# Performance work log

Measured on AMD Instinct MI355X. Metric: run time of the kernel, lower is better.

Reference implementation:

```python
import jax, jax.numpy as jnp
import numpy as np

B, S, D, H = 2, 2048, 1024, 16
Dh = D // H
EPS = 1e-6


def _layernorm(x, alpha, beta):
    # torch.std is unbiased (ddof=1); module divides by (std + eps)
    m = jnp.mean(x, axis=-1, keepdims=True)
    var = jnp.sum((x - m) ** 2, axis=-1, keepdims=True) / (x.shape[-1] - 1)
    return alpha * (x - m) / (jnp.sqrt(var) + EPS) + beta


def setup_inputs() -> dict:
    key = jax.random.key(0)
    ks = jax.random.split(key, 12)
    sc = 0.02
    return {
        "x": jax.random.normal(ks[0], (B, S, D), jnp.float32),
        "src_mask": jnp.ones((B, 1, S), jnp.int32),
        # per-head q/k/v projections stacked over heads: [H, D, Dh]
        "Wq": jax.random.normal(ks[1], (H, D, Dh), jnp.float32) * sc,
        "bq": jnp.zeros((H, Dh), jnp.float32),
        "Wk": jax.random.normal(ks[2], (H, D, Dh), jnp.float32) * sc,
        "bk": jnp.zeros((H, Dh), jnp.float32),
        "Wv": jax.random.normal(ks[3], (H, D, Dh), jnp.float32) * sc,
        "bv": jnp.zeros((H, Dh), jnp.float32),
        # FFN: D -> 4D -> D
        "W1": jax.random.normal(ks[4], (D, 4 * D), jnp.float32) * sc,
        "b1": jnp.zeros((4 * D,), jnp.float32),
        "W2": jax.random.normal(ks[5], (4 * D, D), jnp.float32) * sc,
        "b2": jnp.zeros((D,), jnp.float32),
        # two LayerNorms (residual connections)
        "alpha1": jnp.ones((D,), jnp.float32),
        "beta1": jnp.zeros((D,), jnp.float32),
        "alpha2": jnp.ones((D,), jnp.float32),
        "beta2": jnp.zeros((D,), jnp.float32),
    }


def _encoder_block(x, src_mask, Wq, bq, Wk, bk, Wv, bv, W1, b1, W2, b2,
                   alpha1, beta1, alpha2, beta2):
    # --- multi-head self-attention (all heads vectorized) ---
    q = jnp.einsum('bsd,hde->bhse', x, Wq) + bq[None, :, None, :]
    k = jnp.einsum('bsd,hde->bhse', x, Wk) + bk[None, :, None, :]
    v = jnp.einsum('bsd,hde->bhse', x, Wv) + bv[None, :, None, :]
    wei = jnp.einsum('bhse,bhte->bhst', q, k) * (Dh ** -0.5)  # [B,H,S,S]
    wei = jnp.where(src_mask[:, None, :, :] == 0, -jnp.inf, wei)
    wei = jax.nn.softmax(wei, axis=-1)
    attn = jnp.einsum('bhst,bhte->bhse', wei, v)  # [B,H,S,Dh]
    attn = attn.transpose(0, 2, 1, 3).reshape(x.shape[0], x.shape[1], D)
    # NOTE: original module never applies its output projection (self.pro unused)
    # residual 1: x + norm(sublayer(x))
    x = x + _layernorm(attn, alpha1, beta1)
    # --- feed-forward ---
    h = jax.nn.relu(x @ W1 + b1)
    ffn = h @ W2 + b2
    x = x + _layernorm(ffn, alpha2, beta2)
    return x


def reference(x, src_mask, Wq, bq, Wk, bk, Wv, bv, W1, b1, W2, b2,
              alpha1, beta1, alpha2, beta2):
    return _encoder_block(x, src_mask, Wq, bq, Wk, bk, Wv, bv,
                          W1, b1, W2, b2, alpha1, beta1, alpha2, beta2)
```

## Files before the change

### kernel.cpp

```cpp
#include <hip/hip_runtime.h>


#define DEV __device__ __forceinline__

typedef unsigned short u16;
typedef unsigned int u32;
typedef __attribute__((ext_vector_type(8))) short bfrag;
typedef __attribute__((ext_vector_type(8))) __bf16 bf16x8;
typedef __attribute__((ext_vector_type(2))) __bf16 bf16x2_t;
typedef __attribute__((ext_vector_type(4))) unsigned int u32x4;
typedef __attribute__((ext_vector_type(4))) float facc;
typedef __attribute__((ext_vector_type(16))) float facc16;

DEV float bf2f(u16 u) {
  unsigned int x = ((unsigned int)u) << 16;
  return __builtin_bit_cast(float, x);
}
DEV u16 f2bf(float f) {
  unsigned int x = __builtin_bit_cast(unsigned int, f);
  x += 0x7fffu + ((x >> 16) & 1u);
  return (u16)(x >> 16);
}

DEV void gl2lds16(const u16* g, u16* l) {
  auto gp = (const __attribute__((address_space(1))) unsigned int*)(g);
  auto lp = (__attribute__((address_space(3))) unsigned int*)(l);
  __builtin_amdgcn_global_load_lds(gp, lp, 16, 0, 0);
}

DEV facc mfma16(bfrag a, bfrag b, facc c) {
  return __builtin_amdgcn_mfma_f32_16x16x32_bf16(
      __builtin_bit_cast(bf16x8, a), __builtin_bit_cast(bf16x8, b), c, 0, 0, 0);
}

DEV facc16 mfma32(bfrag a, bfrag b, facc16 c) {
  return __builtin_amdgcn_mfma_f32_32x32x16_bf16(
      __builtin_bit_cast(bf16x8, a), __builtin_bit_cast(bf16x8, b), c, 0, 0, 0);
}

DEV u32 pk2(float a, float b) {
  bf16x2_t v;
  v[0] = (__bf16)a;
  v[1] = (__bf16)b;
  return __builtin_bit_cast(u32, v);
}

DEV void pswap(u32& a, u32& b) {
  asm volatile("v_permlane32_swap_b32 %0, %1" : "+v"(a), "+v"(b));
}

__global__ __launch_bounds__(256) void prep_kernel(
    const float* __restrict__ Wq, const float* __restrict__ Wk,
    const float* __restrict__ Wv, u16* __restrict__ WqkvT,
    const float* __restrict__ W1, u16* __restrict__ W1T,
    const float* __restrict__ W2, u16* __restrict__ W2T,
    const float* __restrict__ x, u16* __restrict__ xb) {
  __shared__ float tile[32][33];
  const int job = blockIdx.x;
  const int tr = threadIdx.x >> 5, tc = threadIdx.x & 31;

  if (job >= 11264) {
    const int i = (job - 11264) * 1024 + threadIdx.x * 4;
    const float4 v = *(const float4*)(x + i);
    ushort4 o;
    o.x = f2bf(v.x); o.y = f2bf(v.y); o.z = f2bf(v.z); o.w = f2bf(v.w);
    *(ushort4*)(xb + i) = o;
    return;
  }

  const float* in;
  u16* out;
  int C, R, c0, r0;
  if (job < 3072) {
    const int z = job >> 6, rem = job & 63;
    const int which = z >> 4, h = z & 15;
    in = ((which == 0) ? Wq : (which == 1) ? Wk : Wv) + (size_t)h * 1024 * 64;
    out = WqkvT + ((size_t)which * 1024 + h * 64) * 1024;
    C = 64; R = 1024;
    c0 = (rem & 1) * 32; r0 = (rem >> 1) * 32;
  } else if (job < 7168) {
    const int rem = job - 3072;
    in = W1; out = W1T; C = 4096; R = 1024;
    c0 = (rem & 127) * 32; r0 = (rem >> 7) * 32;
  } else {
    const int rem = job - 7168;
    in = W2; out = W2T; C = 1024; R = 4096;
    c0 = (rem & 31) * 32; r0 = (rem >> 5) * 32;
  }
#pragma unroll
  for (int k = 0; k < 4; k++)
    tile[tr + 8 * k][tc] = in[(size_t)(r0 + tr + 8 * k) * C + c0 + tc];
  __syncthreads();
#pragma unroll
  for (int k = 0; k < 4; k++)
    out[(size_t)(c0 + tr + 8 * k) * R + r0 + tc] = f2bf(tile[tc][tr + 8 * k]);
}

template <int MODE>
__global__ __launch_bounds__(512, 2) void gemm256(
    const u16* __restrict__ A, int lda, const u16* __restrict__ Bt, int ldb,
    int M, int N, int K,
    const float* __restrict__ bias0, const float* __restrict__ bias1,
    const float* __restrict__ bias2,
    void* __restrict__ out0, void* __restrict__ out1, void* __restrict__ out2) {
  __shared__ __align__(16) u16 As[2][256 * 64];
  __shared__ __align__(16) u16 Bs[2][256 * 64];
  const int tid = threadIdx.x;
  const int lane = tid & 63;
  const int wave = tid >> 6;
  const int laneM = lane & 15, quad = lane >> 4;
  const int kx = laneM & 7;
  const int m0 = blockIdx.x * 256, n0 = blockIdx.y * 256;
  const int wm = wave & 1, wn = wave >> 1;

  const u16* Ab = A;
  const u16* Bb = Bt;
  if (MODE == 3) {
    Ab += (size_t)blockIdx.z * K;
    Bb += (size_t)blockIdx.z * K;
  }

  int srow[4], skl[4];
#pragma unroll
  for (int c = 0; c < 4; c++) {
    const int slot = wave * 256 + c * 64 + lane;
    srow[c] = slot >> 3;
    skl[c] = ((slot & 7) ^ (srow[c] & 7)) * 8;
  }

  auto stage = [&](int X, int t) {
    const u16* Asrc = Ab + (size_t)t * 64;
    const u16* Bsrc = Bb + (size_t)t * 64;
#pragma unroll
    for (int c = 0; c < 4; c++)
      gl2lds16(Asrc + (size_t)(m0 + srow[c]) * lda + skl[c],
               As[X] + (size_t)(wave * 256 + c * 64) * 8);
#pragma unroll
    for (int c = 0; c < 4; c++)
      gl2lds16(Bsrc + (size_t)(n0 + srow[c]) * ldb + skl[c],
               Bs[X] + (size_t)(wave * 256 + c * 64) * 8);
  };

  facc acc[8][4] = {};

  const int NT = K >> 6;
  stage(0, 0);

  for (int t = 0; t < NT; ++t) {
    const int cur = t & 1;
    if (t + 1 < NT) {
      stage(cur ^ 1, t + 1);
      asm volatile("s_waitcnt vmcnt(8)" ::: "memory");
    } else {
      asm volatile("s_waitcnt vmcnt(0)" ::: "memory");
    }
    __builtin_amdgcn_s_barrier();

    const u16* as = As[cur];
    const u16* bs = Bs[cur];
#pragma unroll
    for (int k32 = 0; k32 < 2; ++k32) {
      bfrag af[8], bf[4];
#pragma unroll
      for (int i = 0; i < 8; i++) {
        const int row = wm * 128 + i * 16 + laneM;
        af[i] = *(const bfrag*)(as + row * 64 + (((k32 * 4 + quad) ^ kx) * 8));
      }
#pragma unroll
      for (int j = 0; j < 4; j++) {
        const int row = wn * 64 + j * 16 + laneM;
        bf[j] = *(const bfrag*)(bs + row * 64 + (((k32 * 4 + quad) ^ kx) * 8));
      }
#pragma unroll
      for (int i = 0; i < 8; i++)
#pragma unroll
        for (int j = 0; j < 4; j++)
          acc[i][j] = mfma16(af[i], bf[j], acc[i][j]);
    }
    __builtin_amdgcn_s_barrier();
  }

#pragma unroll
  for (int i = 0; i < 8; i++) {
#pragma unroll
    for (int j = 0; j < 4; j++) {
      const int col = n0 + wn * 64 + j * 16 + laneM;
      const int row0 = m0 + wm * 128 + i * 16 + quad * 4;
      if (MODE == 0) {
        const int which = col >> 10, c = col & 1023;
        const float* bp = (which == 0) ? bias0 : (which == 1) ? bias1 : bias2;
        u16* op = (u16*)((which == 0) ? out0 : (which == 1) ? out1 : out2);
        const float bb = bp[c];
        const int b = row0 >> 11, s0 = row0 & 2047;
        const int h = c >> 6, e = c & 63;
        if (which == 2) {
          ushort4 pk;
          pk.x = f2bf(acc[i][j][0] + bb);
          pk.y = f2bf(acc[i][j][1] + bb);
          pk.z = f2bf(acc[i][j][2] + bb);
          pk.w = f2bf(acc[i][j][3] + bb);
          *(ushort4*)(op + ((size_t)((b * 16 + h) * 64 + e)) * 2048 + s0) = pk;
        } else {
#pragma unroll
          for (int v = 0; v < 4; v++)
            op[((size_t)(b * 16 + h) * 2048 + s0 + v) * 64 + e] =
                f2bf(acc[i][j][v] + bb);
        }
      } else if (MODE == 1) {
        const float bb = bias0[col];
#pragma unroll
        for (int v = 0; v < 4; v++)
          ((u16*)out0)[(size_t)(row0 + v) * N + col] =
              f2bf(fmaxf(acc[i][j][v] + bb, 0.0f));
      } else {
        const int z = blockIdx.z;
        u16* op = (u16*)((z < 2) ? out0 : out1) + (size_t)(z & 1) * M * N;
#pragma unroll
        for (int v = 0; v < 4; v++)
          op[(size_t)(row0 + v) * N + col] = f2bf(acc[i][j][v]);
      }
    }
  }
}

__global__ __launch_bounds__(256) void attn_kernel(
    const u16* __restrict__ Qb, const u16* __restrict__ Kb,
    const u16* __restrict__ VTg, const int* __restrict__ mask,
    u16* __restrict__ Opart, float* __restrict__ lbuf) {
  __shared__ __align__(16) u16 KT[2][64 * 64];
  __shared__ __align__(16) u16 VS[2][64 * 64];
  __shared__ float MB[1024];
  const int tid = threadIdx.x;
  const int lane = tid & 63;
  const int wave = tid >> 6;
  const int col = lane & 31, hi = lane >> 5;
  const int bh = blockIdx.x, b = bh >> 4, h = bh & 15;
  const int q0 = blockIdx.y * 128;
  const int z = blockIdx.z;
  const int sbase = z * 1024;
  const u16* Qh = Qb + (size_t)bh * 2048 * 64;
  const u16* Kh = Kb + (size_t)bh * 2048 * 64 + (size_t)sbase * 64;
  const u16* Vh = VTg + (size_t)bh * 64 * 2048 + sbase;
  const float SC = 0.125f * 1.4426950408889634f;

  const int q = q0 + wave * 32 + col;
  bfrag qf[4];
#pragma unroll
  for (int ds = 0; ds < 4; ds++)
    qf[ds] = *(const bfrag*)(Qh + (size_t)q * 64 + ds * 16 + 8 * hi);

#pragma unroll
  for (int t = 0; t < 4; t++) {
    const int i = t * 256 + tid;
    MB[i] = mask[b * 2048 + sbase + i] ? 0.0f : -1e30f;
  }

  const int s0 = wave * 128;
  const int sl0 = s0 + lane, sl1 = s0 + 64 + lane;
  const int r0s = sl0 >> 3, c0s = ((sl0 & 7) ^ (r0s & 7)) * 8;
  const int r1s = sl1 >> 3, c1s = ((sl1 & 7) ^ (r1s & 7)) * 8;

  const int kx = col & 7;
  int off4[4];
#pragma unroll
  for (int i = 0; i < 4; i++) off4[i] = ((i * 2 + hi) ^ kx) << 3;

  gl2lds16(Kh + (size_t)r0s * 64 + c0s, KT[0] + (size_t)s0 * 8);
  gl2lds16(Kh + (size_t)r1s * 64 + c1s, KT[0] + (size_t)(s0 + 64) * 8);
  gl2lds16(Vh + (size_t)r0s * 2048 + c0s, VS[0] + (size_t)s0 * 8);
  gl2lds16(Vh + (size_t)r1s * 2048 + c1s, VS[0] + (size_t)(s0 + 64) * 8);
  __syncthreads();

  float lsum = 0.0f;
  facc16 oacc0 = (facc16)0.0f, oacc1 = (facc16)0.0f;

  for (int it = 0; it < 16; ++it) {
    const int t0 = it * 64;
    const int cur = it & 1;
    if (it < 15) {
      const int nxt = cur ^ 1;
      const int t0n = t0 + 64;
      gl2lds16(Kh + (size_t)(t0n + r0s) * 64 + c0s, KT[nxt] + (size_t)s0 * 8);
      gl2lds16(Kh + (size_t)(t0n + r1s) * 64 + c1s,
               KT[nxt] + (size_t)(s0 + 64) * 8);
      gl2lds16(Vh + (size_t)r0s * 2048 + t0n + c0s, VS[nxt] + (size_t)s0 * 8);
      gl2lds16(Vh + (size_t)r1s * 2048 + t0n + c1s,
               VS[nxt] + (size_t)(s0 + 64) * 8);
      asm volatile("s_waitcnt vmcnt(4)" ::: "memory");
    } else {
      asm volatile("s_waitcnt vmcnt(0)" ::: "memory");
    }
    __builtin_amdgcn_s_barrier();

    const u16* kb = KT[cur];
    const u16* vb = VS[cur];
#pragma unroll
    for (int tile = 0; tile < 2; tile++) {
      facc16 sacc = (facc16)0.0f;
#pragma unroll
      for (int ds = 0; ds < 4; ds++) {
        bfrag kf = *(const bfrag*)(kb + (tile * 32 + col) * 64 + off4[ds]);
        sacc = mfma32(kf, qf[ds], sacc);
      }
      u32 w[8];
#pragma unroll
      for (int g = 0; g < 4; g++) {
        const float4 mg = *(const float4*)(MB + t0 + tile * 32 + g * 8 + 4 * hi);
        const float p0 = __builtin_amdgcn_exp2f(fmaf(sacc[g * 4 + 0], SC, mg.x));
        const float p1 = __builtin_amdgcn_exp2f(fmaf(sacc[g * 4 + 1], SC, mg.y));
        const float p2 = __builtin_amdgcn_exp2f(fmaf(sacc[g * 4 + 2], SC, mg.z));
        const float p3 = __builtin_amdgcn_exp2f(fmaf(sacc[g * 4 + 3], SC, mg.w));
        lsum += (p0 + p1) + (p2 + p3);
        w[g * 2 + 0] = pk2(p0, p1);
        w[g * 2 + 1] = pk2(p2, p3);
      }
      pswap(w[0], w[2]);
      pswap(w[1], w[3]);
      pswap(w[4], w[6]);
      pswap(w[5], w[7]);
#pragma unroll
      for (int sub = 0; sub < 2; sub++) {
        u32x4 pv4;
        pv4[0] = w[sub * 4 + 0];
        pv4[1] = w[sub * 4 + 1];
        pv4[2] = w[sub * 4 + 2];
        pv4[3] = w[sub * 4 + 3];
        const bfrag pa = __builtin_bit_cast(bfrag, pv4);
        const int ks = tile * 2 + sub;
        {
          bfrag vf = *(const bfrag*)(vb + (0 * 32 + col) * 64 + off4[ks]);
          oacc0 = mfma32(vf, pa, oacc0);
        }
        {
          bfrag vf = *(const bfrag*)(vb + (1 * 32 + col) * 64 + off4[ks]);
          oacc1 = mfma32(vf, pa, oacc1);
        }
      }
    }
    __builtin_amdgcn_s_barrier();
  }

  const float l = lsum + __shfl_xor(lsum, 32, 64);
  if (hi == 0) lbuf[((size_t)(z * 32 + bh)) * 2048 + q] = l;

  u16* dst = Opart + (size_t)z * 4096 * 1024 +
             ((size_t)(b * 2048 + q)) * 1024 + h * 64;
#pragma unroll
  for (int eh = 0; eh < 2; eh++) {
    const facc16& oa = eh ? oacc1 : oacc0;
#pragma unroll
    for (int g = 0; g < 4; g++) {
      ushort4 pk;
      pk.x = f2bf(oa[g * 4 + 0]);
      pk.y = f2bf(oa[g * 4 + 1]);
      pk.z = f2bf(oa[g * 4 + 2]);
      pk.w = f2bf(oa[g * 4 + 3]);
      *(ushort4*)(dst + eh * 32 + g * 8 + 4 * hi) = pk;
    }
  }
}

__global__ __launch_bounds__(256) void ln_attn(
    const float* __restrict__ base, const u16* __restrict__ Opart,
    const float* __restrict__ lbuf,
    const float* __restrict__ alpha, const float* __restrict__ beta,
    float* __restrict__ outf, u16* __restrict__ outb) {
  __shared__ float red[4];
  const int row = blockIdx.x;
  const int t = threadIdx.x;
  const int b = row >> 11, s = row & 2047;
  const int h = t >> 4;
  const size_t off = (size_t)row * 1024 + t * 4;
  const size_t zstride = (size_t)4096 * 1024;

  const float l0 = lbuf[((size_t)(b * 16 + h)) * 2048 + s];
  const float l1 = lbuf[((size_t)(32 + b * 16 + h)) * 2048 + s];
  const float inv = 1.0f / (l0 + l1);

  const ushort4 o0 = *(const ushort4*)(Opart + off);
  const ushort4 o1 = *(const ushort4*)(Opart + zstride + off);
  float4 yv;
  yv.x = (bf2f(o0.x) + bf2f(o1.x)) * inv;
  yv.y = (bf2f(o0.y) + bf2f(o1.y)) * inv;
  yv.z = (bf2f(o0.z) + bf2f(o1.z)) * inv;
  yv.w = (bf2f(o0.w) + bf2f(o1.w)) * inv;

  float sm = yv.x + yv.y + yv.z + yv.w;
#pragma unroll
  for (int o = 1; o < 64; o <<= 1) sm += __shfl_xor(sm, o, 64);
  if ((t & 63) == 0) red[t >> 6] = sm;
  __syncthreads();
  const float mean = (red[0] + red[1] + red[2] + red[3]) * (1.0f / 1024.0f);
  __syncthreads();

  const float d0 = yv.x - mean, d1 = yv.y - mean, d2 = yv.z - mean, d3 = yv.w - mean;
  float ss = d0 * d0 + d1 * d1 + d2 * d2 + d3 * d3;
#pragma unroll
  for (int o = 1; o < 64; o <<= 1) ss += __shfl_xor(ss, o, 64);
  if ((t & 63) == 0) red[t >> 6] = ss;
  __syncthreads();
  const float var = (red[0] + red[1] + red[2] + red[3]) * (1.0f / 1023.0f);
  const float rstd = 1.0f / (sqrtf(var) + 1e-6f);

  const float4 bv = *(const float4*)(base + off);
  const float4 av = *(const float4*)(alpha + (size_t)t * 4);
  const float4 ev = *(const float4*)(beta + (size_t)t * 4);

  float4 ov;
  ov.x = bv.x + av.x * d0 * rstd + ev.x;
  ov.y = bv.y + av.y * d1 * rstd + ev.y;
  ov.z = bv.z + av.z * d2 * rstd + ev.z;
  ov.w = bv.w + av.w * d3 * rstd + ev.w;
  *(float4*)(outf + off) = ov;
  ushort4 ob;
  ob.x = f2bf(ov.x); ob.y = f2bf(ov.y); ob.z = f2bf(ov.z); ob.w = f2bf(ov.w);
  *(ushort4*)(outb + off) = ob;
}

__global__ __launch_bounds__(256) void ln_res2(
    const float* __restrict__ base, const u16* __restrict__ parts0,
    const u16* __restrict__ parts1, const float* __restrict__ biasv,
    const float* __restrict__ alpha, const float* __restrict__ beta,
    float* __restrict__ outf) {
  __shared__ float red[4];
  const int row = blockIdx.x;
  const int t = threadIdx.x;
  const size_t off = (size_t)row * 1024 + t * 4;
  const size_t stride = (size_t)4096 * 1024;

  float4 yv = *(const float4*)(biasv + (size_t)t * 4);
#pragma unroll
  for (int zi = 0; zi < 2; zi++) {
    const ushort4 pz = *(const ushort4*)(parts0 + zi * stride + off);
    yv.x += bf2f(pz.x); yv.y += bf2f(pz.y);
    yv.z += bf2f(pz.z); yv.w += bf2f(pz.w);
  }
#pragma unroll
  for (int zi = 0; zi < 2; zi++) {
    const ushort4 pz = *(const ushort4*)(parts1 + zi * stride + off);
    yv.x += bf2f(pz.x); yv.y += bf2f(pz.y);
    yv.z += bf2f(pz.z); yv.w += bf2f(pz.w);
  }

  float s = yv.x + yv.y + yv.z + yv.w;
#pragma unroll
  for (int o = 1; o < 64; o <<= 1) s += __shfl_xor(s, o, 64);
  if ((t & 63) == 0) red[t >> 6] = s;
  __syncthreads();
  const float mean = (red[0] + red[1] + red[2] + red[3]) * (1.0f / 1024.0f);
  __syncthreads();

  const float d0 = yv.x - mean, d1 = yv.y - mean, d2 = yv.z - mean, d3 = yv.w - mean;
  float ss = d0 * d0 + d1 * d1 + d2 * d2 + d3 * d3;
#pragma unroll
  for (int o = 1; o < 64; o <<= 1) ss += __shfl_xor(ss, o, 64);
  if ((t & 63) == 0) red[t >> 6] = ss;
  __syncthreads();
  const float var = (red[0] + red[1] + red[2] + red[3]) * (1.0f / 1023.0f);
  const float rstd = 1.0f / (sqrtf(var) + 1e-6f);

  const float4 bv = *(const float4*)(base + off);
  const float4 av = *(const float4*)(alpha + (size_t)t * 4);
  const float4 ev = *(const float4*)(beta + (size_t)t * 4);

  float4 ov;
  ov.x = bv.x + av.x * d0 * rstd + ev.x;
  ov.y = bv.y + av.y * d1 * rstd + ev.y;
  ov.z = bv.z + av.z * d2 * rstd + ev.z;
  ov.w = bv.w + av.w * d3 * rstd + ev.w;
  *(float4*)(outf + off) = ov;
}

extern "C" void kernel_launch(void* const* d_in, const int* in_sizes, int n_in,
                              void* d_out, int out_size, void* d_ws,
                              size_t ws_size, hipStream_t stream) {
  const float* x  = (const float*)d_in[0];
  const int* mask = (const int*)d_in[1];
  const float* Wq = (const float*)d_in[2];
  const float* bq = (const float*)d_in[3];
  const float* Wk = (const float*)d_in[4];
  const float* bk = (const float*)d_in[5];
  const float* Wv = (const float*)d_in[6];
  const float* bv = (const float*)d_in[7];
  const float* W1 = (const float*)d_in[8];
  const float* b1 = (const float*)d_in[9];
  const float* W2 = (const float*)d_in[10];
  const float* b2 = (const float*)d_in[11];
  const float* alpha1 = (const float*)d_in[12];
  const float* beta1  = (const float*)d_in[13];
  const float* alpha2 = (const float*)d_in[14];
  const float* beta2  = (const float*)d_in[15];
  float* out = (float*)d_out;

  char* p = (char*)d_ws;
  u16* xb      = (u16*)p;  p += (size_t)4096 * 1024 * 2;
  u16* WqkvT   = (u16*)p;  p += (size_t)3072 * 1024 * 2;
  u16* W1T     = (u16*)p;  p += (size_t)4096 * 1024 * 2;
  u16* W2T     = (u16*)p;  p += (size_t)1024 * 4096 * 2;
  u16* Qbuf    = (u16*)p;  p += (size_t)32 * 2048 * 64 * 2;
  u16* Kbuf    = (u16*)p;  p += (size_t)32 * 2048 * 64 * 2;
  u16* Vbuf    = (u16*)p;  p += (size_t)32 * 2048 * 64 * 2;
  u16* attnp   = (u16*)p;  p += (size_t)2 * 4096 * 1024 * 2;
  float* lbuf  = (float*)p; p += (size_t)2 * 32 * 2048 * 4;
  float* x1f   = (float*)p; p += (size_t)4096 * 1024 * 4;
  u16* x1b     = (u16*)p;  p += (size_t)4096 * 1024 * 2;
  u16* hbuf    = (u16*)p;  p += (size_t)4096 * 4096 * 2;
  u16* ffnp    = (u16*)p;  p += (size_t)2 * 4096 * 1024 * 2;

  prep_kernel<<<15360, 256, 0, stream>>>(Wq, Wk, Wv, WqkvT, W1, W1T, W2, W2T,
                                         x, xb);

  gemm256<0><<<dim3(16, 12), 512, 0, stream>>>(
      xb, 1024, WqkvT, 1024, 4096, 3072, 1024, bq, bk, bv, Qbuf, Kbuf, Vbuf);

  attn_kernel<<<dim3(32, 16, 2), 256, 0, stream>>>(Qbuf, Kbuf, Vbuf, mask,
                                                   attnp, lbuf);

  ln_attn<<<4096, 256, 0, stream>>>(x, attnp, lbuf, alpha1, beta1, x1f, x1b);

  gemm256<1><<<dim3(16, 16), 512, 0, stream>>>(
      x1b, 1024, W1T, 1024, 4096, 4096, 1024, b1, nullptr, nullptr,
      hbuf, nullptr, nullptr);

  gemm256<3><<<dim3(16, 4, 4), 512, 0, stream>>>(
      hbuf, 4096, W2T, 4096, 4096, 1024, 1024, nullptr, nullptr, nullptr,
      ffnp, attnp, nullptr);

  ln_res2<<<4096, 256, 0, stream>>>(x1f, ffnp, attnp, b2, alpha2, beta2, out);
}
```

Before: 312.8 us.

## Split K/V wait so softmax overlaps V tile load

The attention loop now waits only for the K tile before computing QK^T scores and the exp2 softmax for both 32-column tiles. It then waits for the V tile with a second barrier before the PV MFMAs. This hides part of the V load latency behind the score computation. In exchange it adds a barrier per iteration and keeps two score accumulators and two sets of packed probabilities live, which raises register pressure. The vmcnt counts assume a fixed issue order for the gl2lds16 instructions.

After: 321.9 us. +2.9%, slower.

```diff
diff --git a/kernel.cpp b/kernel.cpp
--- a/kernel.cpp
+++ b/kernel.cpp
@@ -277,7 +277,8 @@
   for (int it = 0; it < 16; ++it) {
     const int t0 = it * 64;
     const int cur = it & 1;
-    if (it < 15) {
+    const bool pf = (it < 15);
+    if (pf) {
       const int nxt = cur ^ 1;
       const int t0n = t0 + 64;
       gl2lds16(Kh + (size_t)(t0n + r0s) * 64 + c0s, KT[nxt] + (size_t)s0 * 8);
@@ -286,14 +287,17 @@
       gl2lds16(Vh + (size_t)r0s * 2048 + t0n + c0s, VS[nxt] + (size_t)s0 * 8);
       gl2lds16(Vh + (size_t)r1s * 2048 + t0n + c1s,
                VS[nxt] + (size_t)(s0 + 64) * 8);
-      asm volatile("s_waitcnt vmcnt(4)" ::: "memory");
+      asm volatile("s_waitcnt vmcnt(6)" ::: "memory");
     } else {
-      asm volatile("s_waitcnt vmcnt(0)" ::: "memory");
+      asm volatile("s_waitcnt vmcnt(2)" ::: "memory");
     }
     __builtin_amdgcn_s_barrier();
 
     const u16* kb = KT[cur];
     const u16* vb = VS[cur];
+
+    facc16 sacc_[2];
+    u32 w_[2][8];
 #pragma unroll
     for (int tile = 0; tile < 2; tile++) {
       facc16 sacc = (facc16)0.0f;
@@ -302,29 +306,40 @@
         bfrag kf = *(const bfrag*)(kb + (tile * 32 + col) * 64 + off4[ds]);
         sacc = mfma32(kf, qf[ds], sacc);
       }
-      u32 w[8];
+      sacc_[tile] = sacc;
+    }
+#pragma unroll
+    for (int tile = 0; tile < 2; tile++) {
 #pragma unroll
       for (int g = 0; g < 4; g++) {
         const float4 mg = *(const float4*)(MB + t0 + tile * 32 + g * 8 + 4 * hi);
-        const float p0 = __builtin_amdgcn_exp2f(fmaf(sacc[g * 4 + 0], SC, mg.x));
-        const float p1 = __builtin_amdgcn_exp2f(fmaf(sacc[g * 4 + 1], SC, mg.y));
-        const float p2 = __builtin_amdgcn_exp2f(fmaf(sacc[g * 4 + 2], SC, mg.z));
-        const float p3 = __builtin_amdgcn_exp2f(fmaf(sacc[g * 4 + 3], SC, mg.w));
+        const float p0 = __builtin_amdgcn_exp2f(fmaf(sacc_[tile][g * 4 + 0], SC, mg.x));
+        const float p1 = __builtin_amdgcn_exp2f(fmaf(sacc_[tile][g * 4 + 1], SC, mg.y));
+        const float p2 = __builtin_amdgcn_exp2f(fmaf(sacc_[tile][g * 4 + 2], SC, mg.z));
+        const float p3 = __builtin_amdgcn_exp2f(fmaf(sacc_[tile][g * 4 + 3], SC, mg.w));
         lsum += (p0 + p1) + (p2 + p3);
-        w[g * 2 + 0] = pk2(p0, p1);
-        w[g * 2 + 1] = pk2(p2, p3);
+        w_[tile][g * 2 + 0] = pk2(p0, p1);
+        w_[tile][g * 2 + 1] = pk2(p2, p3);
       }
-      pswap(w[0], w[2]);
-      pswap(w[1], w[3]);
-      pswap(w[4], w[6]);
-      pswap(w[5], w[7]);
+      pswap(w_[tile][0], w_[tile][2]);
+      pswap(w_[tile][1], w_[tile][3]);
+      pswap(w_[tile][4], w_[tile][6]);
+      pswap(w_[tile][5], w_[tile][7]);
+    }
+
+    if (pf) asm volatile("s_waitcnt vmcnt(4)" ::: "memory");
+    else    asm volatile("s_waitcnt vmcnt(0)" ::: "memory");
+    __builtin_amdgcn_s_barrier();
+
+#pragma unroll
+    for (int tile = 0; tile < 2; tile++) {
 #pragma unroll
       for (int sub = 0; sub < 2; sub++) {
         u32x4 pv4;
-        pv4[0] = w[sub * 4 + 0];
-        pv4[1] = w[sub * 4 + 1];
-        pv4[2] = w[sub * 4 + 2];
-        pv4[3] = w[sub * 4 + 3];
+        pv4[0] = w_[tile][sub * 4 + 0];
+        pv4[1] = w_[tile][sub * 4 + 1];
+        pv4[2] = w_[tile][sub * 4 + 2];
+        pv4[3] = w_[tile][sub * 4 + 3];
         const bfrag pa = __builtin_bit_cast(bfrag, pv4);
         const int ks = tile * 2 + sub;
         {
```
